# Optimization experiments

Measured on AMD Instinct MI355X. Metric: run time of the kernel, lower is better.

The kernel has to match this reference:

```python
import jax, jax.numpy as jnp
import numpy as np

N_HEADS, D_MODEL, D_HEAD, N_CTX = 16, 2048, 128, 2048
BATCH, SEQ = 2, 2048
ATTN_SCALE = float(np.sqrt(D_HEAD))
IGNORE = -100000.0


def setup_inputs() -> dict:
    key = jax.random.key(0)
    ks = jax.random.split(key, 6)
    init = 0.02
    return {
        "residual": jax.random.normal(ks[0], (BATCH, SEQ, D_MODEL), dtype=jnp.float32),
        "x": jax.random.normal(ks[1], (BATCH, SEQ, D_MODEL), dtype=jnp.float32),
        "W_Q": jax.random.normal(ks[2], (N_HEADS, D_MODEL, D_HEAD), dtype=jnp.float32) * init,
        "W_K": jax.random.normal(ks[3], (N_HEADS, D_MODEL, D_HEAD), dtype=jnp.float32) * init,
        "W_V": jax.random.normal(ks[4], (N_HEADS, D_MODEL, D_HEAD), dtype=jnp.float32) * init,
        "W_O": jax.random.normal(ks[5], (N_HEADS, D_HEAD, D_MODEL), dtype=jnp.float32) * init,
        "b_Q": jnp.zeros((N_HEADS, D_HEAD), dtype=jnp.float32),
        "b_K": jnp.zeros((N_HEADS, D_HEAD), dtype=jnp.float32),
        "b_V": jnp.zeros((N_HEADS, D_HEAD), dtype=jnp.float32),
        "b_O": jnp.zeros((D_MODEL,), dtype=jnp.float32),
    }


def reference(residual, x, W_Q, W_K, W_V, W_O, b_Q, b_K, b_V, b_O):
    # use_split_qkv_input=False: QKV all read from residual
    q = jnp.einsum('bpm,hmd->bphd', residual, W_Q) + b_Q  # [b, pos, h, d_head]
    k = jnp.einsum('bpm,hmd->bphd', residual, W_K) + b_K
    v = jnp.einsum('bpm,hmd->bphd', residual, W_V) + b_V
    attn_scores = jnp.einsum('bqhd,bkhd->bhqk', q, k) / ATTN_SCALE  # [b, h, q, k]
    key_len = attn_scores.shape[-1]
    mask = jnp.tril(jnp.ones((key_len, key_len), dtype=bool))  # causal mask [q, k]
    attn_scores = jnp.where(mask, attn_scores, IGNORE)
    pattern = jax.nn.softmax(attn_scores, axis=-1)
    z = jnp.einsum('bkhd,bhqk->bqhd', v, pattern)
    out = jnp.einsum('bphd,hdm->bpm', z, W_O) + b_O
    return (residual, out)
```

## Files before the change

### kernel.cpp

```cpp
#include <hip/hip_runtime.h>
#include <hip/hip_bf16.h>

typedef __attribute__((ext_vector_type(8))) short bf16x8;
typedef __attribute__((ext_vector_type(4))) float f32x4;

#define N_HEADS 16
#define D_MODEL 2048
#define D_HEAD  128
#define SEQ     2048
#define BATCH   2
#define HD      (N_HEADS * D_HEAD)
#define QSCALE  0.08838834764831845f

__device__ inline __hip_bfloat16 to_bf16(float v) { return __float2bfloat16(v); }
__device__ inline __hip_bfloat16 to_bf16(__hip_bfloat16 v) { return v; }

typedef __attribute__((address_space(3))) unsigned lds_u32_t;
typedef __attribute__((address_space(1))) unsigned glb_u32_t;
__device__ inline void async16(void* l, const void* g) {
    __builtin_amdgcn_global_load_lds((const glb_u32_t*)g, (lds_u32_t*)l, 16, 0, 0);
}

__global__ __launch_bounds__(256) void cvt_dual(
    const float4* __restrict__ in, float4* __restrict__ o32,
    __hip_bfloat16* __restrict__ obf, long n4)
{
    for (long i = (long)blockIdx.x * blockDim.x + threadIdx.x; i < n4;
         i += (long)gridDim.x * blockDim.x) {
        float4 v = in[i];
        o32[i] = v;
        union { __hip_bfloat16 b[4]; uint2 u; } p;
        p.b[0] = __float2bfloat16(v.x);
        p.b[1] = __float2bfloat16(v.y);
        p.b[2] = __float2bfloat16(v.z);
        p.b[3] = __float2bfloat16(v.w);
        *(uint2*)(obf + 4 * i) = p.u;
    }
}

template <typename Tin>
__global__ __launch_bounds__(256) void transpose_to_bf16(
    const Tin* __restrict__ in, __hip_bfloat16* __restrict__ out,
    int R, int C, long in_rs, long in_bs, long out_bs)
{
    __shared__ Tin tile[64][65];
    const Tin* src = in + (long)blockIdx.z * in_bs;
    __hip_bfloat16* dst = out + (long)blockIdx.z * out_bs;
    const int c0 = blockIdx.x * 64, r0 = blockIdx.y * 64;
    const int t = threadIdx.x;
    const int tr = t >> 4;
    const int tc = (t & 15) * 4;
#pragma unroll
    for (int i = 0; i < 4; i++) {
        int r = tr + i * 16;
#pragma unroll
        for (int j = 0; j < 4; j++)
            tile[r][tc + j] = src[(long)(r0 + r) * in_rs + c0 + tc + j];
    }
    __syncthreads();
#pragma unroll
    for (int i = 0; i < 4; i++) {
        int c = tr + i * 16;
#pragma unroll
        for (int j = 0; j < 4; j++)
            dst[(long)(c0 + c) * R + r0 + tc + j] = to_bf16(tile[tc + j][c]);
    }
}

__global__ __launch_bounds__(256) void transpose_w3(
    const float* __restrict__ Wq, const float* __restrict__ Wk,
    const float* __restrict__ Wv, __hip_bfloat16* __restrict__ out)
{
    __shared__ float tile[64][65];
    const int z = blockIdx.z;
    const int w = z >> 4, hh = z & 15;
    const float* src = (w == 0 ? Wq : (w == 1 ? Wk : Wv))
                       + (long)hh * D_MODEL * D_HEAD;
    __hip_bfloat16* dst = out + (long)w * D_MODEL * D_MODEL
                          + (long)hh * D_HEAD * D_MODEL;
    const int c0 = blockIdx.x * 64, r0 = blockIdx.y * 64;
    const int t = threadIdx.x;
    const int tr = t >> 4;
    const int tc = (t & 15) * 4;
#pragma unroll
    for (int i = 0; i < 4; i++) {
        int r = tr + i * 16;
#pragma unroll
        for (int j = 0; j < 4; j++)
            tile[r][tc + j] = src[(long)(r0 + r) * D_HEAD + c0 + tc + j];
    }
    __syncthreads();
#pragma unroll
    for (int i = 0; i < 4; i++) {
        int c = tr + i * 16;
#pragma unroll
        for (int j = 0; j < 4; j++)
            dst[(long)(c0 + c) * D_MODEL + r0 + tc + j] = __float2bfloat16(tile[tc + j][c]);
    }
}

__global__ __launch_bounds__(256) void transpose_v(
    const __hip_bfloat16* __restrict__ Vb, __hip_bfloat16* __restrict__ Vt)
{
    __shared__ __hip_bfloat16 tile[64][65];
    const int z = blockIdx.z;
    const int bb = z >> 4, hh = z & 15;
    const __hip_bfloat16* src = Vb + (long)bb * SEQ * D_MODEL + hh * D_HEAD;
    __hip_bfloat16* dst = Vt + ((long)bb * N_HEADS + hh) * (long)D_HEAD * SEQ;
    const int c0 = blockIdx.x * 64, r0 = blockIdx.y * 64;
    const int t = threadIdx.x;
    const int tr = t >> 4;
    const int tc = (t & 15) * 4;
#pragma unroll
    for (int i = 0; i < 4; i++) {
        int r = tr + i * 16;
#pragma unroll
        for (int j = 0; j < 4; j++)
            tile[r][tc + j] = src[(long)(r0 + r) * D_MODEL + c0 + tc + j];
    }
    __syncthreads();
#pragma unroll
    for (int i = 0; i < 4; i++) {
        int c = tr + i * 16;
#pragma unroll
        for (int j = 0; j < 4; j++)
            dst[(long)(c0 + c) * SEQ + r0 + tc + j] = tile[tc + j][c];
    }
}

__device__ inline void store_out(__hip_bfloat16* p, float v) { *p = __float2bfloat16(v); }
__device__ inline void store_out(float* p, float v) { *p = v; }

template <typename OutT>
__global__ __launch_bounds__(256) void gemm_qkv(
    const __hip_bfloat16* __restrict__ A,
    const __hip_bfloat16* __restrict__ WTbase,
    const float* __restrict__ bQ, const float* bK, const float* bV,
    OutT* __restrict__ Cbase,
    int M, int N, int K, long wstride, long cstride, float scale0)
{
    __shared__ __align__(16) __hip_bfloat16 As[128 * 32];
    __shared__ __align__(16) __hip_bfloat16 Bs[128 * 32];
    const int z = blockIdx.z;
    const __hip_bfloat16* Bt = WTbase + (long)z * wstride;
    const float* bias = (z == 0) ? bQ : ((z == 1) ? bK : bV);
    OutT* C = Cbase + (long)z * cstride;
    const float outscale = (z == 0) ? scale0 : 1.0f;

    const int tid = threadIdx.x;
    const int lane = tid & 63, wave = tid >> 6;
    const int l15 = lane & 15, quad = lane >> 4;
    const int wr = wave >> 1, wc = wave & 1;
    const int m0 = blockIdx.y * 128, n0 = blockIdx.x * 128;

    const short* Ap = (const short*)A;
    const short* Bp = (const short*)Bt;

    f32x4 acc[4][4] = {};

    for (int k0 = 0; k0 < K; k0 += 32) {
        __syncthreads();
#pragma unroll
        for (int i = 0; i < 2; i++) {
            int e = i * 256 + tid;
            int row = e >> 2, ch = e & 3;
            async16((char*)As + (i * 256 + wave * 64) * 16,
                    Ap + (long)(m0 + row) * K + k0 + ch * 8);
            async16((char*)Bs + (i * 256 + wave * 64) * 16,
                    Bp + (long)(n0 + row) * K + k0 + ch * 8);
        }
        __syncthreads();

        bf16x8 af[4], bfr[4];
#pragma unroll
        for (int t = 0; t < 4; t++) {
            af[t]  = *(const bf16x8*)((const short*)As + (wr * 64 + t * 16 + l15) * 32 + quad * 8);
            bfr[t] = *(const bf16x8*)((const short*)Bs + (wc * 64 + t * 16 + l15) * 32 + quad * 8);
        }
#pragma unroll
        for (int i = 0; i < 4; i++)
#pragma unroll
            for (int j = 0; j < 4; j++)
                acc[i][j] = __builtin_amdgcn_mfma_f32_16x16x32_bf16(af[i], bfr[j], acc[i][j], 0, 0, 0);
    }

    const int mw = m0 + wr * 64, nw = n0 + wc * 64;
#pragma unroll
    for (int i = 0; i < 4; i++) {
#pragma unroll
        for (int j = 0; j < 4; j++) {
            int n = nw + j * 16 + l15;
            float bv = bias[n];
#pragma unroll
            for (int r = 0; r < 4; r++) {
                int m = mw + i * 16 + quad * 4 + r;
                store_out(&C[(long)m * N + n], (acc[i][j][r] + bv) * outscale);
            }
        }
    }
}

template <typename OutT>
__global__ __launch_bounds__(256, 2) void gemm128(
    const __hip_bfloat16* __restrict__ A,
    const __hip_bfloat16* __restrict__ WTbase,
    const float* __restrict__ bQ, const float* bK, const float* bV,
    OutT* __restrict__ Cbase,
    int N, int K, long wstride, long cstride, float scale0,
    int nx, int ny)
{
    __shared__ __align__(16) short lds[2][2][128 * 64];

    const int tid = threadIdx.x;
    const int lane = tid & 63;
    const int wave = tid >> 6;
    const int l15 = lane & 15, quad = lane >> 4, l7 = lane & 7;
    const int wm = wave >> 1, wn = wave & 1;

    const int nwg = gridDim.x;
    const int orig = blockIdx.x;
    const int wg = (orig & 7) * (nwg >> 3) + (orig >> 3);
    const int nxy = nx * ny;
    const int z = wg / nxy;
    const int rem = wg - z * nxy;
    const int by = rem / nx;
    const int bx = rem - by * nx;
    const int m0 = by * 128, n0 = bx * 128;

    const short* Ap = (const short*)A;
    const short* Bp = (const short*)WTbase + (long)z * wstride;

    const int rsub = lane >> 3;
    const int c0 = (lane & 7) ^ rsub;

    auto stage = [&](int bf, int reg, const short* gbase, int kt) {
        char* base = (char*)&lds[bf][reg][0];
        const short* g = gbase + (long)kt * 64;
#pragma unroll
        for (int s = 0; s < 4; s++) {
            int row = (s * 4 + wave) * 8 + rsub;
            async16(base + (s * 4 + wave) * 1024, g + (long)row * K + c0 * 8);
        }
    };

    const short* Agbl = Ap + (long)m0 * K;
    const short* Bgbl = Bp + (long)n0 * K;

    const int NT = K >> 6;

    stage(0, 0, Agbl, 0); stage(0, 1, Bgbl, 0);
    stage(1, 0, Agbl, 1);
    asm volatile("s_waitcnt vmcnt(4)" ::: "memory");
    __builtin_amdgcn_s_barrier();

    f32x4 acc[4][4] = {};
    const int ar0 = wm * 64;
    const int br0 = wn * 64;

#pragma unroll 2
    for (int u = 0; u < NT; ++u) {
        asm volatile("" ::: "memory");
        const int bf = u & 1, bo = bf ^ 1;
        const short* la = &lds[bf][0][0];
        const short* lb = &lds[bf][1][0];

        bf16x8 a[4][2], b0[2][2], b1[2][2];

#pragma unroll
        for (int fm = 0; fm < 4; fm++)
#pragma unroll
            for (int kk = 0; kk < 2; kk++)
                a[fm][kk] = *(const bf16x8*)(la + (ar0 + fm * 16 + l15) * 64
                                             + (((kk * 4 + quad) ^ l7) * 8));
#pragma unroll
        for (int fn = 0; fn < 2; fn++)
#pragma unroll
            for (int kk = 0; kk < 2; kk++)
                b0[fn][kk] = *(const bf16x8*)(lb + (br0 + fn * 16 + l15) * 64
                                              + (((kk * 4 + quad) ^ l7) * 8));
        if (u + 1 < NT) stage(bo, 1, Bgbl, u + 1);
        __builtin_amdgcn_s_barrier();
        asm volatile("s_waitcnt lgkmcnt(0)" ::: "memory");
        __builtin_amdgcn_sched_barrier(0);
        __builtin_amdgcn_s_setprio(1);
#pragma unroll
        for (int fm = 0; fm < 4; fm++)
#pragma unroll
            for (int fn = 0; fn < 2; fn++)
#pragma unroll
                for (int kk = 0; kk < 2; kk++)
                    acc[fm][fn] = __builtin_amdgcn_mfma_f32_16x16x32_bf16(
                        a[fm][kk], b0[fn][kk], acc[fm][fn], 0, 0, 0);
        __builtin_amdgcn_s_setprio(0);
        __builtin_amdgcn_s_barrier();

#pragma unroll
        for (int fn = 0; fn < 2; fn++)
#pragma unroll
            for (int kk = 0; kk < 2; kk++)
                b1[fn][kk] = *(const bf16x8*)(lb + (br0 + 32 + fn * 16 + l15) * 64
                                              + (((kk * 4 + quad) ^ l7) * 8));
        if (u + 2 < NT) stage(bf, 0, Agbl, u + 2);
        __builtin_amdgcn_s_barrier();
        asm volatile("s_waitcnt lgkmcnt(0)" ::: "memory");
        __builtin_amdgcn_sched_barrier(0);
        __builtin_amdgcn_s_setprio(1);
#pragma unroll
        for (int fm = 0; fm < 4; fm++)
#pragma unroll
            for (int fn = 0; fn < 2; fn++)
#pragma unroll
                for (int kk = 0; kk < 2; kk++)
                    acc[fm][2 + fn] = __builtin_amdgcn_mfma_f32_16x16x32_bf16(
                        a[fm][kk], b1[fn][kk], acc[fm][2 + fn], 0, 0, 0);
        __builtin_amdgcn_s_setprio(0);
        if (u + 2 < NT) {
            asm volatile("s_waitcnt vmcnt(4)" ::: "memory");
        } else if (u + 1 < NT) {
            asm volatile("s_waitcnt vmcnt(0)" ::: "memory");
        }
        __builtin_amdgcn_s_barrier();
    }

    const float* bias = (z == 0) ? bQ : ((z == 1) ? bK : bV);
    OutT* C = Cbase + (long)z * cstride;
    const float outscale = (z == 0) ? scale0 : 1.0f;
#pragma unroll
    for (int mi = 0; mi < 4; mi++) {
#pragma unroll
        for (int nj = 0; nj < 4; nj++) {
            const int n = n0 + wn * 64 + nj * 16 + l15;
            const float bv = bias[n];
#pragma unroll
            for (int r = 0; r < 4; r++) {
                const int m = m0 + wm * 64 + mi * 16 + quad * 4 + r;
                store_out(&C[(long)m * N + n], (acc[mi][nj][r] + bv) * outscale);
            }
        }
    }
}

__global__ __launch_bounds__(512, 4) void attn_fused(
    const __hip_bfloat16* Q,
    const __hip_bfloat16* __restrict__ Kin,
    const __hip_bfloat16* __restrict__ Vt,
    __hip_bfloat16* Z)
{
    __shared__ __align__(16) __hip_bfloat16 Ks[2][64 * 128];
    __shared__ __align__(16) __hip_bfloat16 Vs[128 * 64];
    __shared__ __align__(16) __hip_bfloat16 pbuf[8][16 * 80];

    const int tid = threadIdx.x;
    const int lane = tid & 63, wave = tid >> 6;
    const int l15 = lane & 15, quad = lane >> 4;
    const int wh = wave >> 2;
    const int rr4 = (wave & 3) * 16 + quad * 4;

    const int g0id = blockIdx.x;
    const int qt = (g0id < 256) ? (15 - (g0id & 15)) : (g0id & 15);
    const int hb = ((g0id >> 4) & 15) + ((g0id >> 8) << 4);
    const int b = hb >> 4, h = hb & 15;

    const short* Qp = (const short*)Q;
    const short* Kp = (const short*)Kin;
    const short* Vp = (const short*)Vt;

    bf16x8 aq[4];
#pragma unroll
    for (int ks = 0; ks < 4; ks++)
        aq[ks] = *(const bf16x8*)(Qp + (long)(b * SEQ + qt * 128 + wave * 16 + l15) * HD
                                  + h * D_HEAD + ks * 32 + quad * 8);

    f32x4 o[8] = {};
    float lsum[4] = {};

    const short* pw = (const short*)pbuf[wave];

    auto stageK = [&](int buf, int kt) {
#pragma unroll
        for (int i = 0; i < 2; i++) {
            int e = i * 512 + tid;
            int row = e >> 4, cc = (e & 15) ^ (row & 7);
            async16((char*)&Ks[buf][0] + (size_t)e * 16,
                    Kp + (long)(b * SEQ + kt * 64 + row) * HD + h * D_HEAD + cc * 8);
        }
    };
    auto stageV = [&](int kt) {
#pragma unroll
        for (int i = 0; i < 2; i++) {
            int e = i * 512 + tid;
            int row = e >> 3, cc = (e & 7) ^ (row & 7);
            async16((char*)Vs + (size_t)e * 16,
                    Vp + ((long)(b * N_HEADS + h) * D_HEAD + row) * SEQ + kt * 64 + cc * 8);
        }
    };

    const int ktiles = 2 * qt + 2;
    stageK(0, 0);

    for (int kt = 0; kt < ktiles; kt++) {
        const int buf = kt & 1;
        const bool more = (kt + 1 < ktiles);

        stageV(kt);
        if (more) stageK(buf ^ 1, kt + 1);

        if (more) asm volatile("s_waitcnt vmcnt(4)" ::: "memory");
        else      asm volatile("s_waitcnt vmcnt(2)" ::: "memory");
        __builtin_amdgcn_s_barrier();
        asm volatile("" ::: "memory");

        const bool active = (kt <= 2 * qt + wh);
        f32x4 s[4] = {};
        if (active) {
#pragma unroll
            for (int nt = 0; nt < 4; nt++)
#pragma unroll
                for (int ks = 0; ks < 4; ks++) {
                    bf16x8 bk = *(const bf16x8*)((const short*)&Ks[buf][0] + (nt * 16 + l15) * 128
                                                 + (((ks * 4 + quad) ^ (l15 & 7)) * 8));
                    s[nt] = __builtin_amdgcn_mfma_f32_16x16x32_bf16(aq[ks], bk, s[nt], 0, 0, 0);
                }

            if (kt == 2 * qt + wh) {
#pragma unroll
                for (int nt = 0; nt < 4; nt++)
#pragma unroll
                    for (int r = 0; r < 4; r++) {
                        int kk = nt * 16 + l15;
                        if (kk > rr4 + r) s[nt][r] = -100000.0f;
                    }
            }

#pragma unroll
            for (int nt = 0; nt < 4; nt++)
#pragma unroll
                for (int r = 0; r < 4; r++) {
                    float p = __expf(s[nt][r]);
                    lsum[r] += p;
                    pbuf[wave][(quad * 4 + r) * 80 + nt * 16 + l15] = __float2bfloat16(p);
                }
        }

        if (more) asm volatile("s_waitcnt vmcnt(2)" ::: "memory");
        else      asm volatile("s_waitcnt vmcnt(0)" ::: "memory");
        __builtin_amdgcn_s_barrier();
        asm volatile("" ::: "memory");

        if (active) {
#pragma unroll
            for (int ks2 = 0; ks2 < 2; ks2++) {
                bf16x8 ap = *(const bf16x8*)(pw + l15 * 80 + ks2 * 32 + quad * 8);
#pragma unroll
                for (int tj = 0; tj < 8; tj++) {
                    bf16x8 bv = *(const bf16x8*)((const short*)Vs + (tj * 16 + l15) * 64
                                                 + (((ks2 * 4 + quad) ^ (l15 & 7)) * 8));
                    o[tj] = __builtin_amdgcn_mfma_f32_16x16x32_bf16(ap, bv, o[tj], 0, 0, 0);
                }
            }
        }

        __builtin_amdgcn_s_barrier();
        asm volatile("" ::: "memory");
    }

    float inv[4];
#pragma unroll
    for (int r = 0; r < 4; r++) {
        float v = lsum[r];
#pragma unroll
        for (int ofs = 1; ofs < 16; ofs <<= 1)
            v += __shfl_xor(v, ofs, 64);
        inv[r] = 1.0f / v;
    }
#pragma unroll
    for (int tj = 0; tj < 8; tj++)
#pragma unroll
        for (int r = 0; r < 4; r++) {
            long q = b * SEQ + qt * 128 + wave * 16 + quad * 4 + r;
            Z[q * HD + h * D_HEAD + tj * 16 + l15] = __float2bfloat16(o[tj][r] * inv[r]);
        }
}

extern "C" void kernel_launch(void* const* d_in, const int* in_sizes, int n_in,
                              void* d_out, int out_size, void* d_ws, size_t ws_size,
                              hipStream_t stream)
{
    const float* residual = (const float*)d_in[0];
    const float* W_Q = (const float*)d_in[2];
    const float* W_K = (const float*)d_in[3];
    const float* W_V = (const float*)d_in[4];
    const float* W_O = (const float*)d_in[5];
    const float* b_Q = (const float*)d_in[6];
    const float* b_K = (const float*)d_in[7];
    const float* b_V = (const float*)d_in[8];
    const float* b_O = (const float*)d_in[9];
    float* out = (float*)d_out;

    const long TOK = (long)BATCH * SEQ;
    const long TD = TOK * D_MODEL;
    const long WSZ = (long)D_MODEL * D_MODEL;
    char* ws = (char*)d_ws;
    __hip_bfloat16* Qb = (__hip_bfloat16*)(ws);
    __hip_bfloat16* Kb = (__hip_bfloat16*)(ws + TD * 2);
    __hip_bfloat16* Vb = (__hip_bfloat16*)(ws + TD * 4);
    __hip_bfloat16* Rb = (__hip_bfloat16*)(ws + TD * 6);
    __hip_bfloat16* Vt = Rb;
    __hip_bfloat16* WT = (__hip_bfloat16*)(ws + TD * 8);
    __hip_bfloat16* Zb = Qb;

    const size_t NEED_BIG = (size_t)TD * 8 + (size_t)WSZ * 2 * 3;
    const bool big = ws_size >= NEED_BIG;

    dim3 tB(256);

    cvt_dual<<<2048, tB, 0, stream>>>((const float4*)residual, (float4*)out, Rb, TD / 4);

    if (big) {
        transpose_w3<<<dim3(2, 32, 48), tB, 0, stream>>>(W_Q, W_K, W_V, WT);
        gemm128<__hip_bfloat16><<<dim3(1536), tB, 0, stream>>>(
            Rb, WT, b_Q, b_K, b_V, Qb, D_MODEL, D_MODEL,
            WSZ, TD, QSCALE, D_MODEL / 128, (int)(TOK / 128));
    } else {
        dim3 gridWqkv(D_HEAD / 64, D_MODEL / 64, N_HEADS);
        const float* Wqkv[3] = {W_Q, W_K, W_V};
        const float* bqkv[3] = {b_Q, b_K, b_V};
        dim3 gridG(D_MODEL / 128, (int)(TOK / 128), 1);
        for (int z = 0; z < 3; z++) {
            transpose_to_bf16<float><<<gridWqkv, tB, 0, stream>>>(
                Wqkv[z], WT, D_MODEL, D_HEAD,
                D_HEAD, (long)D_MODEL * D_HEAD, (long)D_HEAD * D_MODEL);
            gemm_qkv<__hip_bfloat16><<<gridG, tB, 0, stream>>>(
                Rb, WT, bqkv[z], bqkv[z], bqkv[z], Qb + (long)z * TD,
                (int)TOK, D_MODEL, D_MODEL, 0, 0, z == 0 ? QSCALE : 1.0f);
        }
    }

    transpose_v<<<dim3(2, 32, 32), tB, 0, stream>>>(Vb, Vt);

    attn_fused<<<dim3(512), dim3(512), 0, stream>>>(Qb, Kb, Vt, Zb);

    dim3 gridWo(D_MODEL / 64, D_MODEL / 64, 1);
    transpose_to_bf16<float><<<gridWo, tB, 0, stream>>>(
        W_O, WT, D_MODEL, D_MODEL, (long)D_MODEL, 0, 0);
    if (big) {
        gemm128<float><<<dim3(512), tB, 0, stream>>>(
            Zb, WT, b_O, b_O, b_O, out + TD, D_MODEL, D_MODEL,
            0, 0, 1.0f, D_MODEL / 128, (int)(TOK / 128));
    } else {
        dim3 gridO(D_MODEL / 128, (int)(TOK / 128), 1);
        gemm_qkv<float><<<gridO, tB, 0, stream>>>(
            Zb, WT, b_O, b_O, b_O, out + TD, (int)TOK, D_MODEL, D_MODEL, 0, 0, 1.0f);
    }
}
```

Measured before the change: 384.6 us.

## Give each attention wave two 16-row query groups with 256-thread blocks

Halves the attention block to 4 waves, each now handling 32 query rows (two 16-row MFMA groups) instead of 16. Every K and V fragment read from LDS is reused for two MFMAs, cutting LDS traffic per FLOP. The per-tile async load counts and waitcnt values are updated to match. Causal masking is generalized with a shift so a wave can span the diagonal. The cost is higher register pressure and fewer waves per block, which may reduce latency hiding.

```diff
diff --git a/kernel.cpp b/kernel.cpp
--- a/kernel.cpp
+++ b/kernel.cpp
@@ -340,7 +340,7 @@
     }
 }
 
-__global__ __launch_bounds__(512, 4) void attn_fused(
+__global__ __launch_bounds__(256, 2) void attn_fused(
     const __hip_bfloat16* Q,
     const __hip_bfloat16* __restrict__ Kin,
     const __hip_bfloat16* __restrict__ Vt,
@@ -348,13 +348,12 @@
 {
     __shared__ __align__(16) __hip_bfloat16 Ks[2][64 * 128];
     __shared__ __align__(16) __hip_bfloat16 Vs[128 * 64];
-    __shared__ __align__(16) __hip_bfloat16 pbuf[8][16 * 80];
+    __shared__ __align__(16) __hip_bfloat16 pbuf[4][32 * 80];
 
     const int tid = threadIdx.x;
     const int lane = tid & 63, wave = tid >> 6;
     const int l15 = lane & 15, quad = lane >> 4;
-    const int wh = wave >> 2;
-    const int rr4 = (wave & 3) * 16 + quad * 4;
+    const int hw = wave >> 1;
 
     const int g0id = blockIdx.x;
     const int qt = (g0id < 256) ? (15 - (g0id & 15)) : (g0id & 15);
@@ -365,21 +364,23 @@
     const short* Kp = (const short*)Kin;
     const short* Vp = (const short*)Vt;
 
-    bf16x8 aq[4];
-#pragma unroll
-    for (int ks = 0; ks < 4; ks++)
-        aq[ks] = *(const bf16x8*)(Qp + (long)(b * SEQ + qt * 128 + wave * 16 + l15) * HD
-                                  + h * D_HEAD + ks * 32 + quad * 8);
-
-    f32x4 o[8] = {};
-    float lsum[4] = {};
+    bf16x8 aq[2][4];
+#pragma unroll
+    for (int g = 0; g < 2; g++)
+#pragma unroll
+        for (int ks = 0; ks < 4; ks++)
+            aq[g][ks] = *(const bf16x8*)(Qp + (long)(b * SEQ + qt * 128 + wave * 32 + g * 16 + l15) * HD
+                                         + h * D_HEAD + ks * 32 + quad * 8);
+
+    f32x4 o[2][8] = {};
+    float lsum[2][4] = {};
 
     const short* pw = (const short*)pbuf[wave];
 
     auto stageK = [&](int buf, int kt) {
 #pragma unroll
-        for (int i = 0; i < 2; i++) {
-            int e = i * 512 + tid;
+        for (int i = 0; i < 4; i++) {
+            int e = i * 256 + tid;
             int row = e >> 4, cc = (e & 15) ^ (row & 7);
             async16((char*)&Ks[buf][0] + (size_t)e * 16,
                     Kp + (long)(b * SEQ + kt * 64 + row) * HD + h * D_HEAD + cc * 8);
@@ -387,8 +388,8 @@
     };
     auto stageV = [&](int kt) {
 #pragma unroll
-        for (int i = 0; i < 2; i++) {
-            int e = i * 512 + tid;
+        for (int i = 0; i < 4; i++) {
+            int e = i * 256 + tid;
             int row = e >> 3, cc = (e & 7) ^ (row & 7);
             async16((char*)Vs + (size_t)e * 16,
                     Vp + ((long)(b * N_HEADS + h) * D_HEAD + row) * SEQ + kt * 64 + cc * 8);
@@ -405,44 +406,51 @@
         stageV(kt);
         if (more) stageK(buf ^ 1, kt + 1);
 
-        if (more) asm volatile("s_waitcnt vmcnt(4)" ::: "memory");
-        else      asm volatile("s_waitcnt vmcnt(2)" ::: "memory");
+        if (more) asm volatile("s_waitcnt vmcnt(8)" ::: "memory");
+        else      asm volatile("s_waitcnt vmcnt(4)" ::: "memory");
         __builtin_amdgcn_s_barrier();
         asm volatile("" ::: "memory");
 
-        const bool active = (kt <= 2 * qt + wh);
-        f32x4 s[4] = {};
+        const bool active = (kt <= 2 * qt + hw);
         if (active) {
+            f32x4 s[2][4] = {};
 #pragma unroll
             for (int nt = 0; nt < 4; nt++)
 #pragma unroll
                 for (int ks = 0; ks < 4; ks++) {
                     bf16x8 bk = *(const bf16x8*)((const short*)&Ks[buf][0] + (nt * 16 + l15) * 128
                                                  + (((ks * 4 + quad) ^ (l15 & 7)) * 8));
-                    s[nt] = __builtin_amdgcn_mfma_f32_16x16x32_bf16(aq[ks], bk, s[nt], 0, 0, 0);
+                    s[0][nt] = __builtin_amdgcn_mfma_f32_16x16x32_bf16(aq[0][ks], bk, s[0][nt], 0, 0, 0);
+                    s[1][nt] = __builtin_amdgcn_mfma_f32_16x16x32_bf16(aq[1][ks], bk, s[1][nt], 0, 0, 0);
                 }
 
-            if (kt == 2 * qt + wh) {
+            if (kt >= 2 * qt) {
+                const int shift = (kt - 2 * qt) * 64;
+#pragma unroll
+                for (int g = 0; g < 2; g++)
+#pragma unroll
+                    for (int nt = 0; nt < 4; nt++)
+#pragma unroll
+                        for (int r = 0; r < 4; r++) {
+                            int lr = wave * 32 + g * 16 + quad * 4 + r - shift;
+                            int kk = nt * 16 + l15;
+                            if (kk > lr) s[g][nt][r] = -100000.0f;
+                        }
+            }
+
+#pragma unroll
+            for (int g = 0; g < 2; g++)
 #pragma unroll
                 for (int nt = 0; nt < 4; nt++)
 #pragma unroll
                     for (int r = 0; r < 4; r++) {
-                        int kk = nt * 16 + l15;
-                        if (kk > rr4 + r) s[nt][r] = -100000.0f;
+                        float p = __expf(s[g][nt][r]);
+                        lsum[g][r] += p;
+                        pbuf[wave][(g * 16 + quad * 4 + r) * 80 + nt * 16 + l15] = __float2bfloat16(p);
                     }
-            }
-
-#pragma unroll
-            for (int nt = 0; nt < 4; nt++)
-#pragma unroll
-                for (int r = 0; r < 4; r++) {
-                    float p = __expf(s[nt][r]);
-                    lsum[r] += p;
-                    pbuf[wave][(quad * 4 + r) * 80 + nt * 16 + l15] = __float2bfloat16(p);
-                }
-        }
-
-        if (more) asm volatile("s_waitcnt vmcnt(2)" ::: "memory");
+        }
+
+        if (more) asm volatile("s_waitcnt vmcnt(4)" ::: "memory");
         else      asm volatile("s_waitcnt vmcnt(0)" ::: "memory");
         __builtin_amdgcn_s_barrier();
         asm volatile("" ::: "memory");
@@ -450,12 +458,14 @@
         if (active) {
 #pragma unroll
             for (int ks2 = 0; ks2 < 2; ks2++) {
-                bf16x8 ap = *(const bf16x8*)(pw + l15 * 80 + ks2 * 32 + quad * 8);
+                bf16x8 ap0 = *(const bf16x8*)(pw + (0  + l15) * 80 + ks2 * 32 + quad * 8);
+                bf16x8 ap1 = *(const bf16x8*)(pw + (16 + l15) * 80 + ks2 * 32 + quad * 8);
 #pragma unroll
                 for (int tj = 0; tj < 8; tj++) {
                     bf16x8 bv = *(const bf16x8*)((const short*)Vs + (tj * 16 + l15) * 64
                                                  + (((ks2 * 4 + quad) ^ (l15 & 7)) * 8));
-                    o[tj] = __builtin_amdgcn_mfma_f32_16x16x32_bf16(ap, bv, o[tj], 0, 0, 0);
+                    o[0][tj] = __builtin_amdgcn_mfma_f32_16x16x32_bf16(ap0, bv, o[0][tj], 0, 0, 0);
+                    o[1][tj] = __builtin_amdgcn_mfma_f32_16x16x32_bf16(ap1, bv, o[1][tj], 0, 0, 0);
                 }
             }
         }
@@ -464,22 +474,25 @@
         asm volatile("" ::: "memory");
     }
 
-    float inv[4];
-#pragma unroll
-    for (int r = 0; r < 4; r++) {
-        float v = lsum[r];
-#pragma unroll
-        for (int ofs = 1; ofs < 16; ofs <<= 1)
-            v += __shfl_xor(v, ofs, 64);
-        inv[r] = 1.0f / v;
-    }
-#pragma unroll
-    for (int tj = 0; tj < 8; tj++)
+#pragma unroll
+    for (int g = 0; g < 2; g++) {
+        float inv[4];
 #pragma unroll
         for (int r = 0; r < 4; r++) {
-            long q = b * SEQ + qt * 128 + wave * 16 + quad * 4 + r;
-            Z[q * HD + h * D_HEAD + tj * 16 + l15] = __float2bfloat16(o[tj][r] * inv[r]);
-        }
+            float v = lsum[g][r];
+#pragma unroll
+            for (int ofs = 1; ofs < 16; ofs <<= 1)
+                v += __shfl_xor(v, ofs, 64);
+            inv[r] = 1.0f / v;
+        }
+#pragma unroll
+        for (int tj = 0; tj < 8; tj++)
+#pragma unroll
+            for (int r = 0; r < 4; r++) {
+                long q = b * SEQ + qt * 128 + wave * 32 + g * 16 + quad * 4 + r;
+                Z[q * HD + h * D_HEAD + tj * 16 + l15] = __float2bfloat16(o[g][tj][r] * inv[r]);
+            }
+    }
 }
 
 extern "C" void kernel_launch(void* const* d_in, const int* in_sizes, int n_in,
@@ -538,7 +551,7 @@
 
     transpose_v<<<dim3(2, 32, 32), tB, 0, stream>>>(Vb, Vt);
 
-    attn_fused<<<dim3(512), dim3(512), 0, stream>>>(Qb, Kb, Vt, Zb);
+    attn_fused<<<dim3(512), dim3(256), 0, stream>>>(Qb, Kb, Vt, Zb);
 
     dim3 gridWo(D_MODEL / 64, D_MODEL / 64, 1);
     transpose_to_bf16<float><<<gridWo, tB, 0, stream>>>(
```

Result: no change. 388.3 us (+1.0%).
